# Kernel tuning notes

Measured on AMD Instinct MI355X. Metric: run time of the kernel, lower is better.

## Reference

```python
import jax, jax.numpy as jnp
import numpy as np

N, E, L, F, M = 512, 2048, 16, 16, 8
HOPS = 2      # egonet radius (k_hop_subgraph num_hops)
H = 128       # WL hash buckets
N_ITER = 3    # WeisfeilerLehman(n_iter=3)
TAU = 0.1     # soft-relabeling temperature


def setup_inputs():
    key = jax.random.key(0)
    k0, k1, k2, k3, k4, k5 = jax.random.split(key, 6)
    labels = jax.random.randint(k0, (N,), 0, L)
    x = jax.nn.one_hot(labels, L, dtype=jnp.float32)
    edge_index = jax.random.randint(k1, (2, E), 0, N)
    # filter adjacencies, built exactly as in GKernel.__init__:
    # symmetric 0/1 with zero diagonal
    A = jax.random.uniform(k2, (F, M, M))
    A = ((A + jnp.swapaxes(A, -1, -2)) > 1.0).astype(jnp.float32)
    A = A * (1.0 - jnp.eye(M, dtype=jnp.float32))
    Xlab = jax.random.randint(k3, (F, M), 0, L)
    X = jax.nn.one_hot(Xlab, L, dtype=jnp.float32)
    # injective label -> bucket embedding (random distinct buckets)
    E0 = jax.nn.one_hot(jax.random.permutation(k4, H)[:L], H, dtype=jnp.float32)
    # random projection used to hash (own-label, neighbor-multiset) signatures
    Rproj = jax.random.normal(k5, (2 * H, H), dtype=jnp.float32)
    return {"x": x, "edge_index": edge_index, "P": A, "X": X, "E0": E0, "Rproj": Rproj}


def _wl_features(c0, nbr_sum, mask, Rproj):
    # soft Weisfeiler-Lehman subtree features: at each iteration the new
    # node label is a hash of (own label, neighbor-label multiset); the
    # graph feature is the concatenated per-iteration label histograms.
    c = c0 * mask[:, None]                       # [n, H]
    feats = [c.sum(0)]
    for _ in range(N_ITER):
        sig = jnp.concatenate([c, nbr_sum(c)], axis=-1)        # [n, 2H]
        c = jax.nn.softmax((sig @ Rproj) / TAU, axis=-1) * mask[:, None]
        feats.append(c.sum(0))
    return jnp.concatenate(feats)                # [(N_ITER+1)*H]


def _max_comp_mask(A):
    # largest connected component via min-label propagation (max_comp)
    comp = jnp.arange(M, dtype=jnp.float32)
    Ab = A > 0
    for _ in range(M):
        nbr_min = jnp.min(jnp.where(Ab, comp[None, :], 1e9), axis=1)
        comp = jnp.minimum(comp, nbr_min)
    ci = comp.astype(jnp.int32)
    counts = jax.ops.segment_sum(jnp.ones(M, jnp.float32), ci, num_segments=M)
    best = jnp.argmax(counts)
    return (ci == best).astype(jnp.float32)


def reference(x, edge_index, P, X, E0, Rproj):
    # symmetrize edges (egonets / WL kernels are undirected)
    src = jnp.concatenate([edge_index[0], edge_index[1]])
    dst = jnp.concatenate([edge_index[1], edge_index[0]])
    # --- k-hop egonet node masks (compute_egonets) : reach[i, j] = 1 iff
    # node j is within HOPS hops of root i ---
    reach = jnp.eye(N, dtype=jnp.float32)
    for _ in range(HOPS):
        agg = jax.ops.segment_sum(reach[:, src].T, dst, num_segments=N).T
        reach = jnp.clip(reach + agg, 0.0, 1.0)
    c0 = x @ E0                                  # initial bucket labels [N, H]

    def ego_feat(mask):
        emask = (mask[src] * mask[dst])[:, None]
        def nbr(c):
            return jax.ops.segment_sum(c[src] * emask, dst, num_segments=N)
        return _wl_features(c0, nbr, mask, Rproj)

    ego_feats = jax.vmap(ego_feat)(reach)        # [N, (N_ITER+1)*H]

    def filt_feat(Af, Xf):
        mask = _max_comp_mask(Af)
        Am = Af * mask[:, None] * mask[None, :]
        return _wl_features(Xf @ E0, lambda c: Am @ c, mask, Rproj)

    filt_feats = jax.vmap(filt_feat)(P, X)       # [F, (N_ITER+1)*H]

    # normalized WL kernel: k(g1,g2)/sqrt(k(g1,g1) k(g2,g2)); sim.T -> [N, F]
    sim = filt_feats @ ego_feats.T               # [F, N]
    nf = jnp.linalg.norm(filt_feats, axis=-1)
    ng = jnp.linalg.norm(ego_feats, axis=-1)
    sim = sim / (nf[:, None] * ng[None, :] + 1e-12)
    return sim.T
```

## Files before the change

kernel.cpp:

```cpp
#include <hip/hip_runtime.h>
#include <hip/hip_bf16.h>

#define NN 512
#define EE 2048
#define LL 16
#define FF 16
#define MM 8
#define HH 128
#define CAP_ROWS 40960
#define MAXD 32
#define TAU_SCALE 14.426950408889634f

typedef __attribute__((ext_vector_type(8))) short bf16x8;
typedef __attribute__((ext_vector_type(8))) unsigned short u16x8;
typedef __attribute__((ext_vector_type(4))) float f32x4;

constexpr size_t OFF_ADJ   = 0;
constexpr size_t SZ_ADJ    = (size_t)NN * 8 * 8;
constexpr size_t OFF_DEG   = OFF_ADJ + SZ_ADJ;
constexpr size_t SZ_DEG    = (size_t)NN * 4;
constexpr size_t OFF_CNT   = OFF_DEG + SZ_DEG;
constexpr size_t SZ_CNT    = (size_t)NN * 4;
constexpr size_t OFF_ROFF  = OFF_CNT + SZ_CNT;
constexpr size_t SZ_ROFF   = (size_t)(NN + 1) * 4 + 12;
constexpr size_t OFF_BUCKN = OFF_ROFF + SZ_ROFF;
constexpr size_t SZ_BUCKN  = (size_t)NN * 4;
constexpr size_t OFF_BUCKF = OFF_BUCKN + SZ_BUCKN;
constexpr size_t SZ_BUCKF  = (size_t)FF * MM * 4;
constexpr size_t OFF_NLST  = ((OFF_BUCKF + SZ_BUCKF + 63) / 64) * 64;
constexpr size_t SZ_NLST   = (size_t)NN * MAXD * 2;
constexpr size_t OFF_CEGO  = OFF_NLST + SZ_NLST;
constexpr size_t SZ_CEGO   = (size_t)CAP_ROWS * 2;
constexpr size_t OFF_NCNT  = OFF_CEGO + SZ_CEGO;
constexpr size_t SZ_NCNT   = (size_t)CAP_ROWS * 2;
constexpr size_t OFF_RBK   = OFF_NCNT + SZ_NCNT;
constexpr size_t SZ_RBK    = (size_t)CAP_ROWS * 2;
constexpr size_t OFF_NBR   = OFF_RBK + SZ_RBK;
constexpr size_t SZ_NBR    = (size_t)CAP_ROWS * MAXD * 2;
constexpr size_t OFF_NBK   = OFF_NBR + SZ_NBR;
constexpr size_t SZ_NBK    = (size_t)CAP_ROWS * MAXD * 2;
constexpr size_t OFF_EGOF  = ((OFF_NBK + SZ_NBK + 63) / 64) * 64;
constexpr size_t SZ_EGOF   = (size_t)NN * 512 * 4;
constexpr size_t OFF_FILTF = OFF_EGOF + SZ_EGOF;
constexpr size_t SZ_FILTF  = (size_t)FF * 512 * 4;
constexpr size_t OFF_FNORM = OFF_FILTF + SZ_FILTF;
constexpr size_t SZ_FNORM  = 64;
constexpr size_t OFF_CA    = ((OFF_FNORM + SZ_FNORM + 255) / 256) * 256;
constexpr size_t SZ_CBUF   = (size_t)CAP_ROWS * HH * 4;
constexpr size_t OFF_CB    = OFF_CA + SZ_CBUF;
constexpr size_t OFF_RT    = OFF_CB + SZ_CBUF;

__device__ __forceinline__ unsigned f2bfbits(float x) {
    unsigned u = __float_as_uint(x);
    return (u + 0x7fffu + ((u >> 16) & 1u)) >> 16;
}
__device__ __forceinline__ float bf2f(unsigned hb) { return __uint_as_float(hb << 16); }

__device__ __forceinline__ int xcd_swz(int bid, int nwg) {
    int cpx = nwg >> 3;
    return (bid & 7) * cpx + (bid >> 3);
}

__global__ __launch_bounds__(256) void k_build(const int* __restrict__ ei,
                                               const float* __restrict__ x,
                                               const float* __restrict__ X,
                                               const float* __restrict__ E0,
                                               const float* __restrict__ Rg,
                                               int* __restrict__ degN,
                                               unsigned short* __restrict__ nbrLstN,
                                               unsigned long long* __restrict__ adj,
                                               int* __restrict__ buckN,
                                               int* __restrict__ buckF,
                                               short* __restrict__ RtH,
                                               short* __restrict__ RtL) {
    int idx = blockIdx.x * blockDim.x + threadIdx.x;
    if (idx < EE) {
        int a = ei[idx], b = ei[EE + idx];
        int p = atomicAdd(&degN[a], 1);
        if (p < MAXD) nbrLstN[(size_t)a * MAXD + p] = (unsigned short)b;
        int q = atomicAdd(&degN[b], 1);
        if (q < MAXD) nbrLstN[(size_t)b * MAXD + q] = (unsigned short)a;
        atomicOr(&adj[(size_t)a * 8 + (b >> 6)], 1ull << (b & 63));
        atomicOr(&adj[(size_t)b * 8 + (a >> 6)], 1ull << (a & 63));
    } else if (idx < EE + NN) {
        int i = idx - EE;
        int lab = 0;
        for (int l = 0; l < LL; ++l) if (x[i * LL + l] > 0.5f) lab = l;
        int b = 0;
        for (int h = 0; h < HH; ++h) if (E0[lab * HH + h] > 0.5f) b = h;
        buckN[i] = b;
    } else if (idx < EE + NN + FF * MM) {
        int fm = idx - EE - NN;
        int lab = 0;
        for (int l = 0; l < LL; ++l) if (X[fm * LL + l] > 0.5f) lab = l;
        int b = 0;
        for (int h = 0; h < HH; ++h) if (E0[lab * HH + h] > 0.5f) b = h;
        buckF[fm] = b;
    } else if (idx < EE + NN + FF * MM + 4096) {
        int pidx = idx - (EE + NN + FF * MM);
        int col = pidx >> 5;
        int kc = (pidx & 31) * 8;
        bf16x8 hv, lv;
#pragma unroll
        for (int j = 0; j < 8; ++j) {
            float xv = Rg[(size_t)(kc + j) * HH + col];
            unsigned hb = f2bfbits(xv);
            hv[j] = (short)hb;
            lv[j] = (short)f2bfbits(xv - bf2f(hb));
        }
        *(bf16x8*)&RtH[(size_t)col * 256 + kc] = hv;
        *(bf16x8*)&RtL[(size_t)col * 256 + kc] = lv;
    }
}

__global__ __launch_bounds__(256, 2) void k_reach(const unsigned long long* __restrict__ adj,
                                                  unsigned long long* __restrict__ bitsR,
                                                  int* __restrict__ count) {
    __shared__ unsigned long long r1[8];
    __shared__ unsigned long long r2[8];
    int i = blockIdx.x, tid = threadIdx.x;
    int t = tid & 63, w = tid >> 6;
    if (tid < 8) {
        unsigned long long v = adj[(size_t)i * 8 + tid];
        if (tid == (i >> 6)) v |= 1ull << (i & 63);
        r1[tid] = v;
        r2[tid] = v;
    }
    __syncthreads();
    unsigned long long p[8] = {0, 0, 0, 0, 0, 0, 0, 0};
#pragma unroll
    for (int rr = 0; rr < 2; ++rr) {
        int rep = 2 * w + rr;
        if ((r1[rep] >> t) & 1ull) {
            int j = t + rep * 64;
#pragma unroll
            for (int w2 = 0; w2 < 8; ++w2) p[w2] |= adj[(size_t)j * 8 + w2];
        }
    }
#pragma unroll
    for (int w2 = 0; w2 < 8; ++w2)
        if (p[w2]) atomicOr(&r2[w2], p[w2]);
    __syncthreads();
    if (tid < 8) bitsR[(size_t)i * 8 + tid] = r2[tid];
    if (tid == 0) {
        int acc = 0;
        for (int w2 = 0; w2 < 8; ++w2) acc += __popcll(r2[w2]);
        count[i] = acc;
    }
}

__global__ __launch_bounds__(64) void k_pack(const unsigned long long* __restrict__ bitsR,
                                             const int* __restrict__ count,
                                             int* __restrict__ rowOff,
                                             const int* __restrict__ degN,
                                             const unsigned short* __restrict__ nbrLstN,
                                             const int* __restrict__ buckN,
                                             unsigned short* __restrict__ nbrRow,
                                             unsigned short* __restrict__ nbrBuck,
                                             unsigned short* __restrict__ nbrCnt,
                                             unsigned short* __restrict__ rowBuck,
                                             unsigned short* __restrict__ cegoG,
                                             float* __restrict__ egoF) {
    __shared__ unsigned long long bits[8];
    __shared__ int wpre[8];
    __shared__ unsigned short cmap_s[NN];
    __shared__ unsigned short nodes_s[NN];
    __shared__ float f0[HH];
    int i = blockIdx.x, t = threadIdx.x;
    int pre = 0;
#pragma unroll
    for (int j = 0; j < 8; ++j) {
        int idx = t * 8 + j;
        int cj = count[idx];
        if (idx < i) pre += cj;
    }
    for (int off = 32; off > 0; off >>= 1) pre += __shfl_xor(pre, off);
    int base = pre;
    if (t == 0) {
        rowOff[i] = base;
        if (i == NN - 1) rowOff[NN] = base + count[i];
    }
    if (t < 8) bits[t] = bitsR[(size_t)i * 8 + t];
    { f0[t] = 0.0f; f0[t + 64] = 0.0f; }
    __syncthreads();
    if (t == 0) {
        int acc = 0;
        for (int w = 0; w < 8; ++w) { wpre[w] = acc; acc += __popcll(bits[w]); }
    }
    __syncthreads();
    int n = count[i];
    if (base >= CAP_ROWS) n = 0;
    else if (base + n > CAP_ROWS) n = CAP_ROWS - base;
    for (int rep = 0; rep < 8; ++rep) {
        int j = t + rep * 64;
        unsigned long long word = bits[rep];
        unsigned short v = 0xFFFFu;
        if ((word >> t) & 1ull) {
            int idx = wpre[rep] + __popcll(word & ((1ull << t) - 1ull));
            if (idx < n) { v = (unsigned short)idx; nodes_s[idx] = (unsigned short)j; }
        }
        cmap_s[j] = v;
    }
    for (int q = 256 + t; q < 512; q += 64) egoF[(size_t)i * 512 + q] = 0.0f;
    __syncthreads();
    for (int m = t; m < n; m += 64) {
        int j = nodes_s[m];
        int b = buckN[j];
        atomicAdd(&f0[b], 1.0f);
        size_t row = (size_t)(base + m);
        rowBuck[row] = (unsigned short)b;
        int dn = degN[j]; if (dn > MAXD) dn = MAXD;
        int cnt = 0;
        for (int e = 0; e < dn; ++e) {
            unsigned short nbNode = nbrLstN[(size_t)j * MAXD + e];
            unsigned short nr = cmap_s[nbNode];
            if (nr != 0xFFFFu && cnt < MAXD) {
                nbrRow[row * MAXD + cnt] = (unsigned short)(base + nr);
                nbrBuck[row * MAXD + cnt] = (unsigned short)buckN[nbNode];
                cnt++;
            }
        }
        nbrCnt[row] = (unsigned short)cnt;
        cegoG[row] = (unsigned short)i;
    }
    __syncthreads();
    if (t < 64) {
        egoF[(size_t)i * 512 + t] = f0[t];
        egoF[(size_t)i * 512 + t + 64] = f0[t + 64];
    }
}

__global__ __launch_bounds__(256, 2) void k_iter1(const int* __restrict__ count,
                                                  const int* __restrict__ rowOff,
                                                  const unsigned short* __restrict__ rowBuck,
                                                  const unsigned short* __restrict__ nbrBuck,
                                                  const unsigned short* __restrict__ nbrCnt,
                                                  const float* __restrict__ Rg,
                                                  float* __restrict__ cOut,
                                                  float* __restrict__ egoF) {
    __shared__ float fs[HH];
    int i = xcd_swz(blockIdx.x, NN);
    int tid = threadIdx.x;
    int base = rowOff[i];
    int n = count[i];
    if (base >= CAP_ROWS) n = 0;
    else if (base + n > CAP_ROWS) n = CAP_ROWS - base;
    if (tid < HH) fs[tid] = 0.0f;
    __syncthreads();
    const float* Rb = Rg + (size_t)HH * HH;
    int col = (tid & 7) * 16;
    float facc[16];
#pragma unroll
    for (int q = 0; q < 16; ++q) facc[q] = 0.0f;
    for (int m = tid >> 3; m < n; m += 32) {
        int gr = base + m;
        float z[16];
        const float* rt = Rg + (size_t)rowBuck[gr] * HH + col;
#pragma unroll
        for (int q = 0; q < 4; ++q) *(float4*)&z[q * 4] = *(const float4*)&rt[q * 4];
        int cnt = nbrCnt[gr];
        const unsigned short* nk = &nbrBuck[(size_t)gr * MAXD];
        for (int eb = 0; eb < cnt; eb += 8) {
            u16x8 nv = *(const u16x8*)&nk[eb];
#pragma unroll
            for (int j = 0; j < 8; ++j) {
                if (eb + j < cnt) {
                    const float* rb = Rb + (size_t)nv[j] * HH + col;
#pragma unroll
                    for (int q = 0; q < 4; ++q) {
                        float4 rv = *(const float4*)&rb[q * 4];
                        z[q * 4 + 0] += rv.x; z[q * 4 + 1] += rv.y;
                        z[q * 4 + 2] += rv.z; z[q * 4 + 3] += rv.w;
                    }
                }
            }
        }
        float mx = z[0];
#pragma unroll
        for (int q = 1; q < 16; ++q) mx = fmaxf(mx, z[q]);
        for (int off = 4; off > 0; off >>= 1) mx = fmaxf(mx, __shfl_xor(mx, off));
        float s = 0.0f;
#pragma unroll
        for (int q = 0; q < 16; ++q) { z[q] = exp2f((z[q] - mx) * TAU_SCALE); s += z[q]; }
        for (int off = 4; off > 0; off >>= 1) s += __shfl_xor(s, off);
        float inv = 1.0f / s;
        float* crow = cOut + (size_t)gr * HH + col;
#pragma unroll
        for (int q = 0; q < 16; ++q) { z[q] *= inv; facc[q] += z[q]; }
#pragma unroll
        for (int q = 0; q < 4; ++q) *(float4*)&crow[q * 4] = *(const float4*)&z[q * 4];
    }
#pragma unroll
    for (int q = 0; q < 16; ++q) atomicAdd(&fs[col + q], facc[q]);
    __syncthreads();
    if (tid < HH) egoF[(size_t)i * 512 + HH + tid] = fs[tid];
}

__global__ __launch_bounds__(64, 1) void k_iter(const float* __restrict__ cur,
                                                float* __restrict__ nxt,
                                                const short* __restrict__ RtH,
                                                const short* __restrict__ RtL,
                                                const int* __restrict__ rowOff,
                                                const unsigned short* __restrict__ nbrRow,
                                                const unsigned short* __restrict__ nbrCnt,
                                                const unsigned short* __restrict__ cegoG,
                                                float* __restrict__ egoF,
                                                int it) {
    int Rtot = rowOff[NN];
    if (Rtot > CAP_ROWS) Rtot = CAP_ROWS;
    int r0 = xcd_swz(blockIdx.x, gridDim.x) * 16;
    if (r0 >= Rtot) return;
    int tid = threadIdx.x;
    int c16 = tid & 15, g = tid >> 4;
    int kb = g * 8;
    int grA = r0 + c16;
    if (grA >= Rtot) grA = Rtot - 1;

    const float* crOwn = &cur[(size_t)grA * HH + kb];
    float4 oc[8];
#pragma unroll
    for (int t = 0; t < 4; ++t) {
        oc[2 * t]     = *(const float4*)&crOwn[t * 32];
        oc[2 * t + 1] = *(const float4*)&crOwn[t * 32 + 4];
    }

    float ua[4][8];
#pragma unroll
    for (int s = 0; s < 4; ++s)
#pragma unroll
        for (int j = 0; j < 8; ++j) ua[s][j] = 0.0f;
    {
        int cnt = nbrCnt[grA];
        const unsigned short* nb = &nbrRow[(size_t)grA * MAXD];
        for (int eb = 0; eb < cnt; eb += 8) {
            u16x8 nv = *(const u16x8*)&nb[eb];
#pragma unroll
            for (int j = 0; j < 8; ++j) {
                if (eb + j < cnt) {
                    const float* cr = &cur[(size_t)nv[j] * HH + kb];
#pragma unroll
                    for (int s = 0; s < 4; ++s) {
                        float4 v0 = *(const float4*)&cr[s * 32];
                        float4 v1 = *(const float4*)&cr[s * 32 + 4];
                        ua[s][0] += v0.x; ua[s][1] += v0.y; ua[s][2] += v0.z; ua[s][3] += v0.w;
                        ua[s][4] += v1.x; ua[s][5] += v1.y; ua[s][6] += v1.z; ua[s][7] += v1.w;
                    }
                }
            }
        }
    }

    f32x4 acc[8];
#pragma unroll
    for (int n = 0; n < 8; ++n) acc[n] = (f32x4)(0.0f);
    const short* bbH = RtH + (size_t)c16 * 256 + kb;
    const short* bbL = RtL + (size_t)c16 * 256 + kb;

#pragma unroll
    for (int s = 0; s < 4; ++s) {
        bf16x8 ahi, alo;
#pragma unroll
        for (int j = 0; j < 8; ++j) {
            float xv = ua[s][j];
            unsigned hb = f2bfbits(xv);
            ahi[j] = (short)hb;
            alo[j] = (short)f2bfbits(xv - bf2f(hb));
        }
        const int t = s + 4;
#pragma unroll
        for (int n = 0; n < 8; ++n) {
            bf16x8 bh = *(const bf16x8*)&bbH[n * 4096 + t * 32];
            bf16x8 bl = *(const bf16x8*)&bbL[n * 4096 + t * 32];
            acc[n] = __builtin_amdgcn_mfma_f32_16x16x32_bf16(ahi, bh, acc[n], 0, 0, 0);
            acc[n] = __builtin_amdgcn_mfma_f32_16x16x32_bf16(ahi, bl, acc[n], 0, 0, 0);
            acc[n] = __builtin_amdgcn_mfma_f32_16x16x32_bf16(alo, bh, acc[n], 0, 0, 0);
        }
    }
    {
#pragma unroll
        for (int t = 0; t < 4; ++t) {
            float4 v0 = oc[2 * t];
            float4 v1 = oc[2 * t + 1];
            float cv[8] = {v0.x, v0.y, v0.z, v0.w, v1.x, v1.y, v1.z, v1.w};
            bf16x8 ahi, alo;
#pragma unroll
            for (int j = 0; j < 8; ++j) {
                unsigned hb = f2bfbits(cv[j]);
                ahi[j] = (short)hb;
                alo[j] = (short)f2bfbits(cv[j] - bf2f(hb));
            }
#pragma unroll
            for (int n = 0; n < 8; ++n) {
                bf16x8 bh = *(const bf16x8*)&bbH[n * 4096 + t * 32];
                bf16x8 bl = *(const bf16x8*)&bbL[n * 4096 + t * 32];
                acc[n] = __builtin_amdgcn_mfma_f32_16x16x32_bf16(ahi, bh, acc[n], 0, 0, 0);
                acc[n] = __builtin_amdgcn_mfma_f32_16x16x32_bf16(ahi, bl, acc[n], 0, 0, 0);
                acc[n] = __builtin_amdgcn_mfma_f32_16x16x32_bf16(alo, bh, acc[n], 0, 0, 0);
            }
        }
    }

    float inv[4];
#pragma unroll
    for (int i = 0; i < 4; ++i) {
        float m = acc[0][i];
#pragma unroll
        for (int n = 1; n < 8; ++n) m = fmaxf(m, acc[n][i]);
        for (int off = 8; off > 0; off >>= 1) m = fmaxf(m, __shfl_xor(m, off));
        float s = 0.0f;
#pragma unroll
        for (int n = 0; n < 8; ++n) {
            float e = exp2f((acc[n][i] - m) * TAU_SCALE);
            acc[n][i] = e; s += e;
        }
        for (int off = 8; off > 0; off >>= 1) s += __shfl_xor(s, off);
        inv[i] = 1.0f / s;
    }

    float fa[8];
#pragma unroll
    for (int n = 0; n < 8; ++n) fa[n] = 0.0f;
    int cege = -1;
#pragma unroll
    for (int i = 0; i < 4; ++i) {
        int gr = r0 + g * 4 + i;
        if (gr < Rtot) {
#pragma unroll
            for (int n = 0; n < 8; ++n) {
                float c = acc[n][i] * inv[i];
                nxt[(size_t)gr * HH + n * 16 + c16] = c;
                acc[n][i] = c;
            }
            int ego = cegoG[gr];
            if (ego != cege) {
                if (cege >= 0) {
#pragma unroll
                    for (int n = 0; n < 8; ++n) {
                        atomicAdd(&egoF[(size_t)cege * 512 + it * HH + n * 16 + c16], fa[n]);
                        fa[n] = 0.0f;
                    }
                }
                cege = ego;
            }
#pragma unroll
            for (int n = 0; n < 8; ++n) fa[n] += acc[n][i];
        }
    }
    if (cege >= 0) {
#pragma unroll
        for (int n = 0; n < 8; ++n)
            atomicAdd(&egoF[(size_t)cege * 512 + it * HH + n * 16 + c16], fa[n]);
    }
}

__global__ __launch_bounds__(256) void k_filt(const float* __restrict__ P,
                                              const int* __restrict__ buckF,
                                              const float* __restrict__ Rg,
                                              float* __restrict__ filtF,
                                              float* __restrict__ fnorm) {
    __shared__ float As[MM][MM];
    __shared__ float Am[MM][MM];
    __shared__ float msk[MM];
    __shared__ float cbuf[2][MM][HH];
    __shared__ float ubuf[MM][HH];
    __shared__ float feats[4 * HH];
    __shared__ float red4[4];
    int f = blockIdx.x, tid = threadIdx.x, wave = tid >> 6, lane = tid & 63;
    if (tid < 64) As[tid >> 3][tid & 7] = P[f * 64 + tid];
    for (int idx = tid; idx < 4 * HH; idx += 256) feats[idx] = 0.f;
    __syncthreads();
    if (tid == 0) {
        float comp[MM];
        for (int m = 0; m < MM; ++m) comp[m] = (float)m;
        for (int it = 0; it < MM; ++it) {
            float nm[MM];
            for (int j = 0; j < MM; ++j) {
                float mn = 1e9f;
                for (int k = 0; k < MM; ++k)
                    if (As[j][k] > 0.f) mn = fminf(mn, comp[k]);
                nm[j] = mn;
            }
            for (int j = 0; j < MM; ++j) comp[j] = fminf(comp[j], nm[j]);
        }
        int cnt[MM], ci[MM];
        for (int m = 0; m < MM; ++m) cnt[m] = 0;
        for (int m = 0; m < MM; ++m) { ci[m] = (int)comp[m]; cnt[ci[m]]++; }
        int best = 0;
        for (int m = 1; m < MM; ++m) if (cnt[m] > cnt[best]) best = m;
        for (int m = 0; m < MM; ++m) msk[m] = (ci[m] == best) ? 1.0f : 0.0f;
    }
    __syncthreads();
    if (tid < 64) Am[tid >> 3][tid & 7] = As[tid >> 3][tid & 7] * msk[tid >> 3] * msk[tid & 7];
    for (int idx = tid; idx < MM * HH; idx += 256) {
        int m = idx >> 7, h = idx & 127;
        cbuf[0][m][h] = (msk[m] > 0.f && h == buckF[f * MM + m]) ? 1.0f : 0.0f;
    }
    __syncthreads();
    if (tid < HH) {
        float s = 0.f;
        for (int m = 0; m < MM; ++m) s += cbuf[0][m][tid];
        feats[tid] = s;
    }
    __syncthreads();
    int cur = 0;
    int h2 = 2 * lane;
    for (int it = 1; it <= 3; ++it) {
#pragma unroll
        for (int jj = 0; jj < 2; ++jj) {
            int d = wave * 2 + jj;
            float u0 = 0.f, u1 = 0.f;
            for (int s = 0; s < MM; ++s) {
                float w = Am[d][s];
                u0 += w * cbuf[cur][s][h2];
                u1 += w * cbuf[cur][s][h2 + 1];
            }
            ubuf[d][h2] = u0;
            ubuf[d][h2 + 1] = u1;
        }
        float a0[2] = {0.f, 0.f}, a1[2] = {0.f, 0.f};
        for (int k = 0; k < HH; ++k) {
            float2 rt = *(const float2*)&Rg[(size_t)k * HH + h2];
            float2 rb = *(const float2*)&Rg[(size_t)(HH + k) * HH + h2];
#pragma unroll
            for (int jj = 0; jj < 2; ++jj) {
                int d = wave * 2 + jj;
                float cd = cbuf[cur][d][k];
                float ud = ubuf[d][k];
                a0[jj] += cd * rt.x + ud * rb.x;
                a1[jj] += cd * rt.y + ud * rb.y;
            }
        }
#pragma unroll
        for (int jj = 0; jj < 2; ++jj) {
            int d = wave * 2 + jj;
            float z0 = a0[jj], z1 = a1[jj];
            float m = fmaxf(z0, z1);
            for (int off = 32; off > 0; off >>= 1) m = fmaxf(m, __shfl_xor(m, off));
            float e0 = exp2f((z0 - m) * TAU_SCALE);
            float e1 = exp2f((z1 - m) * TAU_SCALE);
            float s = e0 + e1;
            for (int off = 32; off > 0; off >>= 1) s += __shfl_xor(s, off);
            float inv = msk[d] / s;
            float c0 = e0 * inv, c1 = e1 * inv;
            cbuf[1 - cur][d][h2] = c0;
            cbuf[1 - cur][d][h2 + 1] = c1;
            atomicAdd(&feats[it * HH + h2], c0);
            atomicAdd(&feats[it * HH + h2 + 1], c1);
        }
        __syncthreads();
        cur = 1 - cur;
    }
    float np = 0.f;
    for (int idx = tid; idx < 4 * HH; idx += 256) {
        float v = feats[idx];
        filtF[(size_t)f * 512 + idx] = v;
        np += v * v;
    }
    for (int off = 32; off > 0; off >>= 1) np += __shfl_xor(np, off);
    if (lane == 0) red4[wave] = np;
    __syncthreads();
    if (tid == 0) fnorm[f] = sqrtf(red4[0] + red4[1] + red4[2] + red4[3]);
}

__global__ __launch_bounds__(64) void k_sim(const float* __restrict__ egoF,
                                            const float* __restrict__ filtF,
                                            const float* __restrict__ fnorm,
                                            float* __restrict__ out) {
    int i = blockIdx.x, lane = threadIdx.x;
    float e[8];
    float ss = 0.f;
#pragma unroll
    for (int r = 0; r < 8; ++r) {
        e[r] = egoF[(size_t)i * 512 + r * 64 + lane];
        ss += e[r] * e[r];
    }
    for (int off = 32; off > 0; off >>= 1) ss += __shfl_xor(ss, off);
    float ng = sqrtf(ss);
    for (int f = 0; f < FF; ++f) {
        float d = 0.f;
#pragma unroll
        for (int r = 0; r < 8; ++r) d += e[r] * filtF[(size_t)f * 512 + r * 64 + lane];
        for (int off = 32; off > 0; off >>= 1) d += __shfl_xor(d, off);
        if (lane == 0) out[i * FF + f] = d / (fnorm[f] * ng + 1e-12f);
    }
}

extern "C" void kernel_launch(void* const* d_in, const int* in_sizes, int n_in,
                              void* d_out, int out_size, void* d_ws, size_t ws_size,
                              hipStream_t stream) {
    (void)in_sizes; (void)n_in; (void)out_size; (void)ws_size;
    const float* x  = (const float*)d_in[0];
    const int*   ei = (const int*)d_in[1];
    const float* P  = (const float*)d_in[2];
    const float* X  = (const float*)d_in[3];
    const float* E0 = (const float*)d_in[4];
    const float* Rg = (const float*)d_in[5];
    float* out = (float*)d_out;
    char* ws = (char*)d_ws;

    unsigned long long* adj   = (unsigned long long*)(ws + OFF_ADJ);
    int* degN   = (int*)(ws + OFF_DEG);
    int* count  = (int*)(ws + OFF_CNT);
    int* rowOff = (int*)(ws + OFF_ROFF);
    int* buckN  = (int*)(ws + OFF_BUCKN);
    int* buckF  = (int*)(ws + OFF_BUCKF);
    unsigned short* nbrLstN = (unsigned short*)(ws + OFF_NLST);
    unsigned short* cego    = (unsigned short*)(ws + OFF_CEGO);
    unsigned short* nbrCnt  = (unsigned short*)(ws + OFF_NCNT);
    unsigned short* rowBuck = (unsigned short*)(ws + OFF_RBK);
    unsigned short* nbrRow  = (unsigned short*)(ws + OFF_NBR);
    unsigned short* nbrBuck = (unsigned short*)(ws + OFF_NBK);
    float* egoF  = (float*)(ws + OFF_EGOF);
    float* filtF = (float*)(ws + OFF_FILTF);
    float* fnorm = (float*)(ws + OFF_FNORM);
    float* cA    = (float*)(ws + OFF_CA);
    float* cB    = (float*)(ws + OFF_CB);
    unsigned long long* bitsR = (unsigned long long*)(ws + OFF_CA);
    short* RtH = (short*)(ws + OFF_RT);
    short* RtL = RtH + (size_t)HH * 256;

    hipMemsetAsync(ws, 0, OFF_CNT, stream);
    k_build<<<(EE + NN + FF * MM + 4096 + 255) / 256, 256, 0, stream>>>(
        ei, x, X, E0, Rg, degN, nbrLstN, adj, buckN, buckF, RtH, RtL);
    k_filt<<<FF, 256, 0, stream>>>(P, buckF, Rg, filtF, fnorm);
    k_reach<<<NN, 256, 0, stream>>>(adj, bitsR, count);
    k_pack<<<NN, 64, 0, stream>>>(bitsR, count, rowOff, degN, nbrLstN, buckN,
                                  nbrRow, nbrBuck, nbrCnt, rowBuck, cego, egoF);
    k_iter1<<<NN, 256, 0, stream>>>(count, rowOff, rowBuck, nbrBuck, nbrCnt, Rg, cB, egoF);
    k_iter<<<CAP_ROWS / 16, 64, 0, stream>>>(cB, cA, RtH, RtL, rowOff, nbrRow, nbrCnt, cego, egoF, 2);
    k_iter<<<CAP_ROWS / 16, 64, 0, stream>>>(cA, cB, RtH, RtL, rowOff, nbrRow, nbrCnt, cego, egoF, 3);
    k_sim<<<NN, 64, 0, stream>>>(egoF, filtF, fnorm, out);
}
```

Before: 303.5 us.

## Coalesce neighbor gathers with half-wave rows and stage MFMA operands in LDS

In k_iter1, each 32-lane half-wave now processes one row, with every lane holding 4 contiguous columns. The neighbor-row gathers become fully coalesced 512-byte reads instead of 8 lanes striding 16 floats each. In k_iter, the own-row and neighbor-sum gathers are also done per row by half-waves with coalesced float4 loads and written to padded LDS tiles. The MFMA fragments are then read back from LDS in the layout they need. This adds shared memory, a barrier and extra shuffle rounds in exchange for better global memory access patterns on the gather-heavy phases.

```diff
diff --git a/kernel.cpp b/kernel.cpp
--- a/kernel.cpp
+++ b/kernel.cpp
@@ -241,6 +241,7 @@
     __shared__ float fs[HH];
     int i = xcd_swz(blockIdx.x, NN);
     int tid = threadIdx.x;
+    int hw = tid >> 5, li = tid & 31;
     int base = rowOff[i];
     int n = count[i];
     if (base >= CAP_ROWS) n = 0;
@@ -248,16 +249,10 @@
     if (tid < HH) fs[tid] = 0.0f;
     __syncthreads();
     const float* Rb = Rg + (size_t)HH * HH;
-    int col = (tid & 7) * 16;
-    float facc[16];
-#pragma unroll
-    for (int q = 0; q < 16; ++q) facc[q] = 0.0f;
-    for (int m = tid >> 3; m < n; m += 32) {
+    float4 facc = make_float4(0.f, 0.f, 0.f, 0.f);
+    for (int m = hw; m < n; m += 8) {
         int gr = base + m;
-        float z[16];
-        const float* rt = Rg + (size_t)rowBuck[gr] * HH + col;
-#pragma unroll
-        for (int q = 0; q < 4; ++q) *(float4*)&z[q * 4] = *(const float4*)&rt[q * 4];
+        float4 z = *(const float4*)&Rg[(size_t)rowBuck[gr] * HH + li * 4];
         int cnt = nbrCnt[gr];
         const unsigned short* nk = &nbrBuck[(size_t)gr * MAXD];
         for (int eb = 0; eb < cnt; eb += 8) {
@@ -265,33 +260,28 @@
 #pragma unroll
             for (int j = 0; j < 8; ++j) {
                 if (eb + j < cnt) {
-                    const float* rb = Rb + (size_t)nv[j] * HH + col;
-#pragma unroll
-                    for (int q = 0; q < 4; ++q) {
-                        float4 rv = *(const float4*)&rb[q * 4];
-                        z[q * 4 + 0] += rv.x; z[q * 4 + 1] += rv.y;
-                        z[q * 4 + 2] += rv.z; z[q * 4 + 3] += rv.w;
-                    }
+                    float4 rv = *(const float4*)&Rb[(size_t)nv[j] * HH + li * 4];
+                    z.x += rv.x; z.y += rv.y; z.z += rv.z; z.w += rv.w;
                 }
             }
         }
-        float mx = z[0];
-#pragma unroll
-        for (int q = 1; q < 16; ++q) mx = fmaxf(mx, z[q]);
-        for (int off = 4; off > 0; off >>= 1) mx = fmaxf(mx, __shfl_xor(mx, off));
-        float s = 0.0f;
-#pragma unroll
-        for (int q = 0; q < 16; ++q) { z[q] = exp2f((z[q] - mx) * TAU_SCALE); s += z[q]; }
-        for (int off = 4; off > 0; off >>= 1) s += __shfl_xor(s, off);
+        float mx = fmaxf(fmaxf(z.x, z.y), fmaxf(z.z, z.w));
+        for (int off = 16; off > 0; off >>= 1) mx = fmaxf(mx, __shfl_xor(mx, off));
+        float e0 = exp2f((z.x - mx) * TAU_SCALE);
+        float e1 = exp2f((z.y - mx) * TAU_SCALE);
+        float e2 = exp2f((z.z - mx) * TAU_SCALE);
+        float e3 = exp2f((z.w - mx) * TAU_SCALE);
+        float s = e0 + e1 + e2 + e3;
+        for (int off = 16; off > 0; off >>= 1) s += __shfl_xor(s, off);
         float inv = 1.0f / s;
-        float* crow = cOut + (size_t)gr * HH + col;
-#pragma unroll
-        for (int q = 0; q < 16; ++q) { z[q] *= inv; facc[q] += z[q]; }
-#pragma unroll
-        for (int q = 0; q < 4; ++q) *(float4*)&crow[q * 4] = *(const float4*)&z[q * 4];
-    }
-#pragma unroll
-    for (int q = 0; q < 16; ++q) atomicAdd(&fs[col + q], facc[q]);
+        z.x = e0 * inv; z.y = e1 * inv; z.z = e2 * inv; z.w = e3 * inv;
+        facc.x += z.x; facc.y += z.y; facc.z += z.z; facc.w += z.w;
+        *(float4*)&cOut[(size_t)gr * HH + li * 4] = z;
+    }
+    atomicAdd(&fs[li * 4 + 0], facc.x);
+    atomicAdd(&fs[li * 4 + 1], facc.y);
+    atomicAdd(&fs[li * 4 + 2], facc.z);
+    atomicAdd(&fs[li * 4 + 3], facc.w);
     __syncthreads();
     if (tid < HH) egoF[(size_t)i * 512 + HH + tid] = fs[tid];
 }
@@ -306,65 +296,60 @@
                                                 const unsigned short* __restrict__ cegoG,
                                                 float* __restrict__ egoF,
                                                 int it) {
+    __shared__ float cT[16][132];
+    __shared__ float uT[16][132];
     int Rtot = rowOff[NN];
     if (Rtot > CAP_ROWS) Rtot = CAP_ROWS;
     int r0 = xcd_swz(blockIdx.x, gridDim.x) * 16;
     if (r0 >= Rtot) return;
     int tid = threadIdx.x;
+    int half = tid >> 5, li = tid & 31;
     int c16 = tid & 15, g = tid >> 4;
     int kb = g * 8;
-    int grA = r0 + c16;
-    if (grA >= Rtot) grA = Rtot - 1;
-
-    const float* crOwn = &cur[(size_t)grA * HH + kb];
-    float4 oc[8];
-#pragma unroll
-    for (int t = 0; t < 4; ++t) {
-        oc[2 * t]     = *(const float4*)&crOwn[t * 32];
-        oc[2 * t + 1] = *(const float4*)&crOwn[t * 32 + 4];
-    }
-
-    float ua[4][8];
-#pragma unroll
-    for (int s = 0; s < 4; ++s)
-#pragma unroll
-        for (int j = 0; j < 8; ++j) ua[s][j] = 0.0f;
-    {
-        int cnt = nbrCnt[grA];
-        const unsigned short* nb = &nbrRow[(size_t)grA * MAXD];
+
+#pragma unroll
+    for (int rp = 0; rp < 8; ++rp) {
+        int m = rp * 2 + half;
+        int gr = r0 + m; if (gr >= Rtot) gr = Rtot - 1;
+        float4 v = *(const float4*)&cur[(size_t)gr * HH + li * 4];
+        *(float4*)&cT[m][li * 4] = v;
+    }
+    for (int rp = 0; rp < 8; ++rp) {
+        int m = rp * 2 + half;
+        int gr = r0 + m; if (gr >= Rtot) gr = Rtot - 1;
+        int cnt = nbrCnt[gr];
+        const unsigned short* nb = &nbrRow[(size_t)gr * MAXD];
+        float4 a = make_float4(0.f, 0.f, 0.f, 0.f);
         for (int eb = 0; eb < cnt; eb += 8) {
             u16x8 nv = *(const u16x8*)&nb[eb];
 #pragma unroll
             for (int j = 0; j < 8; ++j) {
                 if (eb + j < cnt) {
-                    const float* cr = &cur[(size_t)nv[j] * HH + kb];
-#pragma unroll
-                    for (int s = 0; s < 4; ++s) {
-                        float4 v0 = *(const float4*)&cr[s * 32];
-                        float4 v1 = *(const float4*)&cr[s * 32 + 4];
-                        ua[s][0] += v0.x; ua[s][1] += v0.y; ua[s][2] += v0.z; ua[s][3] += v0.w;
-                        ua[s][4] += v1.x; ua[s][5] += v1.y; ua[s][6] += v1.z; ua[s][7] += v1.w;
-                    }
+                    float4 v = *(const float4*)&cur[(size_t)nv[j] * HH + li * 4];
+                    a.x += v.x; a.y += v.y; a.z += v.z; a.w += v.w;
                 }
             }
         }
-    }
+        *(float4*)&uT[m][li * 4] = a;
+    }
+    __syncthreads();
 
     f32x4 acc[8];
 #pragma unroll
     for (int n = 0; n < 8; ++n) acc[n] = (f32x4)(0.0f);
     const short* bbH = RtH + (size_t)c16 * 256 + kb;
     const short* bbL = RtL + (size_t)c16 * 256 + kb;
-
 #pragma unroll
     for (int s = 0; s < 4; ++s) {
+        float uu[8];
+        *(float4*)&uu[0] = *(const float4*)&uT[c16][s * 32 + kb];
+        *(float4*)&uu[4] = *(const float4*)&uT[c16][s * 32 + kb + 4];
         bf16x8 ahi, alo;
 #pragma unroll
         for (int j = 0; j < 8; ++j) {
-            float xv = ua[s][j];
-            unsigned hb = f2bfbits(xv);
+            unsigned hb = f2bfbits(uu[j]);
             ahi[j] = (short)hb;
-            alo[j] = (short)f2bfbits(xv - bf2f(hb));
+            alo[j] = (short)f2bfbits(uu[j] - bf2f(hb));
         }
         const int t = s + 4;
 #pragma unroll
@@ -376,27 +361,25 @@
             acc[n] = __builtin_amdgcn_mfma_f32_16x16x32_bf16(alo, bh, acc[n], 0, 0, 0);
         }
     }
-    {
-#pragma unroll
-        for (int t = 0; t < 4; ++t) {
-            float4 v0 = oc[2 * t];
-            float4 v1 = oc[2 * t + 1];
-            float cv[8] = {v0.x, v0.y, v0.z, v0.w, v1.x, v1.y, v1.z, v1.w};
-            bf16x8 ahi, alo;
-#pragma unroll
-            for (int j = 0; j < 8; ++j) {
-                unsigned hb = f2bfbits(cv[j]);
-                ahi[j] = (short)hb;
-                alo[j] = (short)f2bfbits(cv[j] - bf2f(hb));
-            }
-#pragma unroll
-            for (int n = 0; n < 8; ++n) {
-                bf16x8 bh = *(const bf16x8*)&bbH[n * 4096 + t * 32];
-                bf16x8 bl = *(const bf16x8*)&bbL[n * 4096 + t * 32];
-                acc[n] = __builtin_amdgcn_mfma_f32_16x16x32_bf16(ahi, bh, acc[n], 0, 0, 0);
-                acc[n] = __builtin_amdgcn_mfma_f32_16x16x32_bf16(ahi, bl, acc[n], 0, 0, 0);
-                acc[n] = __builtin_amdgcn_mfma_f32_16x16x32_bf16(alo, bh, acc[n], 0, 0, 0);
-            }
+#pragma unroll
+    for (int t = 0; t < 4; ++t) {
+        float cc[8];
+        *(float4*)&cc[0] = *(const float4*)&cT[c16][t * 32 + kb];
+        *(float4*)&cc[4] = *(const float4*)&cT[c16][t * 32 + kb + 4];
+        bf16x8 ahi, alo;
+#pragma unroll
+        for (int j = 0; j < 8; ++j) {
+            unsigned hb = f2bfbits(cc[j]);
+            ahi[j] = (short)hb;
+            alo[j] = (short)f2bfbits(cc[j] - bf2f(hb));
+        }
+#pragma unroll
+        for (int n = 0; n < 8; ++n) {
+            bf16x8 bh = *(const bf16x8*)&bbH[n * 4096 + t * 32];
+            bf16x8 bl = *(const bf16x8*)&bbL[n * 4096 + t * 32];
+            acc[n] = __builtin_amdgcn_mfma_f32_16x16x32_bf16(ahi, bh, acc[n], 0, 0, 0);
+            acc[n] = __builtin_amdgcn_mfma_f32_16x16x32_bf16(ahi, bl, acc[n], 0, 0, 0);
+            acc[n] = __builtin_amdgcn_mfma_f32_16x16x32_bf16(alo, bh, acc[n], 0, 0, 0);
         }
     }
 
```

Result: slower. 332.5 us (+9.6%).
